# Performance work log

Measured on AMD Instinct MI355X. Metric: run time of the kernel, lower is better.

The kernel has to match this reference:

```python
import jax, jax.numpy as jnp
import numpy as np


def setup_inputs() -> dict:
    key = jax.random.key(0)
    k1, k2, k3 = jax.random.split(key, 3)
    B, S = 4096, 4096
    prediction = jax.random.normal(k1, (B, S), dtype=jnp.float32)
    target = jax.random.normal(k2, (B, S), dtype=jnp.float32)
    mask = jax.random.randint(k3, (B, S), 0, 2, dtype=jnp.int32)
    return {"prediction": prediction, "target": target, "mask": mask}


def reference(prediction, target, mask):
    # Masked MSE with ragged alignment: for each row, the j-th masked position
    # of `prediction` is compared against target[i, j] (i.e. target[:lens[i]]).
    m = mask != 0  # ignored_index == 0
    # rank of each masked position within its row -> index into target row
    rank = jnp.cumsum(m.astype(jnp.int32), axis=1) - 1  # [B, S]
    gathered_target = jnp.take_along_axis(target, jnp.clip(rank, 0, None), axis=1)
    diff2 = jnp.where(m, (prediction - gathered_target) ** 2, jnp.zeros((), prediction.dtype))
    return diff2.sum()  # reduction='sum'
```

## Files before the change

kernel.cpp:

```cpp
#include <hip/hip_runtime.h>

__global__ __launch_bounds__(256) void masked_mse_rows(
    const float* __restrict__ pred,
    const float* __restrict__ target,
    const int*   __restrict__ mask,
    float*       __restrict__ row_sums,
    int S)
{
    const int row  = blockIdx.x;
    const int tid  = threadIdx.x;
    const int lane = tid & 63;
    const int wid  = tid >> 6;

    const float4* __restrict__ p4 = reinterpret_cast<const float4*>(pred + (size_t)row * S);
    const int4*   __restrict__ m4 = reinterpret_cast<const int4*>(mask + (size_t)row * S);
    const float*  __restrict__ trow = target + (size_t)row * S;

    __shared__ int   wsum[4];
    __shared__ float facc[4];

    float acc = 0.0f;
    int running = 0;
    const int nchunk = S >> 10;

    for (int c = 0; c < nchunk; ++c) {
        const int idx = c * 256 + tid;
        const int4   m = m4[idx];
        const float4 p = p4[idx];

        const int b0 = (m.x != 0), b1 = (m.y != 0), b2 = (m.z != 0), b3 = (m.w != 0);
        const int cnt = b0 + b1 + b2 + b3;

        int scan = cnt;
        #pragma unroll
        for (int off = 1; off < 64; off <<= 1) {
            int n = __shfl_up(scan, off, 64);
            if (lane >= off) scan += n;
        }
        if (lane == 63) wsum[wid] = scan;
        __syncthreads();

        int wave_off = 0;
        #pragma unroll
        for (int w = 0; w < 4; ++w) wave_off += (w < wid) ? wsum[w] : 0;
        const int total = wsum[0] + wsum[1] + wsum[2] + wsum[3];

        int r = running + wave_off + (scan - cnt);

        if (b0) { float d = p.x - trow[r]; acc += d * d; ++r; }
        if (b1) { float d = p.y - trow[r]; acc += d * d; ++r; }
        if (b2) { float d = p.z - trow[r]; acc += d * d; ++r; }
        if (b3) { float d = p.w - trow[r]; acc += d * d; ++r; }

        running += total;
        __syncthreads();
    }

    #pragma unroll
    for (int off = 32; off > 0; off >>= 1) acc += __shfl_down(acc, off, 64);
    if (lane == 0) facc[wid] = acc;
    __syncthreads();
    if (tid == 0) row_sums[row] = facc[0] + facc[1] + facc[2] + facc[3];
}

__global__ __launch_bounds__(256) void reduce_rows(
    const float* __restrict__ row_sums, float* __restrict__ out, int n)
{
    const int tid = threadIdx.x;
    float acc = 0.0f;
    for (int i = tid; i < n; i += 256) acc += row_sums[i];
    #pragma unroll
    for (int off = 32; off > 0; off >>= 1) acc += __shfl_down(acc, off, 64);
    __shared__ float facc[4];
    if ((tid & 63) == 0) facc[tid >> 6] = acc;
    __syncthreads();
    if (tid == 0) out[0] = facc[0] + facc[1] + facc[2] + facc[3];
}

extern "C" void kernel_launch(void* const* d_in, const int* in_sizes, int n_in,
                              void* d_out, int out_size, void* d_ws, size_t ws_size,
                              hipStream_t stream) {
    const float* pred   = (const float*)d_in[0];
    const float* target = (const float*)d_in[1];
    const int*   mask   = (const int*)d_in[2];
    float* out = (float*)d_out;
    float* row_sums = (float*)d_ws;

    const int S = 4096;
    const int B = in_sizes[0] / S;

    masked_mse_rows<<<B, 256, 0, stream>>>(pred, target, mask, row_sums, S);
    reduce_rows<<<1, 256, 0, stream>>>(row_sums, out, B);
}
```

Before: 36.15 us.

## Assign one row per wavefront to remove block-level scan barriers

Each 64-lane wavefront now processes a whole row, so the prefix-sum offset comes only from the in-wave shuffle scan plus a broadcast of lane 63. This drops the shared-memory wave-sum exchange and both __syncthreads per chunk. Each lane also loads two float4/int4 vectors per iteration with unroll 2, giving more memory requests in flight. In exchange, each row's scan runs serially within one wave over more iterations, and the grid has a quarter as many blocks.

```diff
diff --git a/kernel.cpp b/kernel.cpp
--- a/kernel.cpp
+++ b/kernel.cpp
@@ -5,31 +5,33 @@
     const float* __restrict__ target,
     const int*   __restrict__ mask,
     float*       __restrict__ row_sums,
-    int S)
+    int S, int B)
 {
-    const int row  = blockIdx.x;
     const int tid  = threadIdx.x;
     const int lane = tid & 63;
     const int wid  = tid >> 6;
+    const int row  = blockIdx.x * 4 + wid;
+    if (row >= B) return;
 
     const float4* __restrict__ p4 = reinterpret_cast<const float4*>(pred + (size_t)row * S);
     const int4*   __restrict__ m4 = reinterpret_cast<const int4*>(mask + (size_t)row * S);
     const float*  __restrict__ trow = target + (size_t)row * S;
 
-    __shared__ int   wsum[4];
-    __shared__ float facc[4];
-
     float acc = 0.0f;
     int running = 0;
-    const int nchunk = S >> 10;
+    const int niter = S >> 9;
 
-    for (int c = 0; c < nchunk; ++c) {
-        const int idx = c * 256 + tid;
-        const int4   m = m4[idx];
-        const float4 p = p4[idx];
+    #pragma unroll 2
+    for (int it = 0; it < niter; ++it) {
+        const int base = it * 128 + lane * 2;
+        const int4   ma = m4[base];
+        const int4   mb = m4[base + 1];
+        const float4 pa = p4[base];
+        const float4 pb = p4[base + 1];
 
-        const int b0 = (m.x != 0), b1 = (m.y != 0), b2 = (m.z != 0), b3 = (m.w != 0);
-        const int cnt = b0 + b1 + b2 + b3;
+        const int b0 = (ma.x != 0), b1 = (ma.y != 0), b2 = (ma.z != 0), b3 = (ma.w != 0);
+        const int b4 = (mb.x != 0), b5 = (mb.y != 0), b6 = (mb.z != 0), b7 = (mb.w != 0);
+        const int cnt = b0 + b1 + b2 + b3 + b4 + b5 + b6 + b7;
 
         int scan = cnt;
         #pragma unroll
@@ -37,30 +39,24 @@
             int n = __shfl_up(scan, off, 64);
             if (lane >= off) scan += n;
         }
-        if (lane == 63) wsum[wid] = scan;
-        __syncthreads();
 
-        int wave_off = 0;
-        #pragma unroll
-        for (int w = 0; w < 4; ++w) wave_off += (w < wid) ? wsum[w] : 0;
-        const int total = wsum[0] + wsum[1] + wsum[2] + wsum[3];
+        int r = running + (scan - cnt);
 
-        int r = running + wave_off + (scan - cnt);
+        if (b0) { float d = pa.x - trow[r]; acc += d * d; ++r; }
+        if (b1) { float d = pa.y - trow[r]; acc += d * d; ++r; }
+        if (b2) { float d = pa.z - trow[r]; acc += d * d; ++r; }
+        if (b3) { float d = pa.w - trow[r]; acc += d * d; ++r; }
+        if (b4) { float d = pb.x - trow[r]; acc += d * d; ++r; }
+        if (b5) { float d = pb.y - trow[r]; acc += d * d; ++r; }
+        if (b6) { float d = pb.z - trow[r]; acc += d * d; ++r; }
+        if (b7) { float d = pb.w - trow[r]; acc += d * d; ++r; }
 
-        if (b0) { float d = p.x - trow[r]; acc += d * d; ++r; }
-        if (b1) { float d = p.y - trow[r]; acc += d * d; ++r; }
-        if (b2) { float d = p.z - trow[r]; acc += d * d; ++r; }
-        if (b3) { float d = p.w - trow[r]; acc += d * d; ++r; }
-
-        running += total;
-        __syncthreads();
+        running += __shfl(scan, 63, 64);
     }
 
     #pragma unroll
     for (int off = 32; off > 0; off >>= 1) acc += __shfl_down(acc, off, 64);
-    if (lane == 0) facc[wid] = acc;
-    __syncthreads();
-    if (tid == 0) row_sums[row] = facc[0] + facc[1] + facc[2] + facc[3];
+    if (lane == 0) row_sums[row] = acc;
 }
 
 __global__ __launch_bounds__(256) void reduce_rows(
@@ -89,6 +85,6 @@
     const int S = 4096;
     const int B = in_sizes[0] / S;
 
-    masked_mse_rows<<<B, 256, 0, stream>>>(pred, target, mask, row_sums, S);
+    masked_mse_rows<<<(B + 3) / 4, 256, 0, stream>>>(pred, target, mask, row_sums, S, B);
     reduce_rows<<<1, 256, 0, stream>>>(row_sums, out, B);
 }
```

Result: slower. 41.38 us (+14.5%).

## Replace per-chunk shuffle scan with ballot/mbcnt prefix and single block sync

Applied to the files above, without the earlier changes.

The row kernel now uses 512 threads that each load two float4/int4 chunks up front. It computes per-lane prefix counts with ballot and mbcnt instead of a 6-step shuffle scan inside a 4-iteration loop. This cuts the number of block-wide barriers from eight to two and issues all loads early for more memory-level parallelism. The final reduction kernel uses 1024 threads with float4 loads. Register pressure rises because two chunks are held per thread, and the occupancy hint of 8 blocks may constrain register allocation.

```diff
diff --git a/kernel.cpp b/kernel.cpp
--- a/kernel.cpp
+++ b/kernel.cpp
@@ -1,80 +1,110 @@
 #include <hip/hip_runtime.h>
 
-__global__ __launch_bounds__(256) void masked_mse_rows(
+__device__ __forceinline__ int lanes_below(unsigned long long m) {
+    return __builtin_amdgcn_mbcnt_hi((unsigned)(m >> 32),
+           __builtin_amdgcn_mbcnt_lo((unsigned)m, 0u));
+}
+
+__global__ __launch_bounds__(512, 8) void masked_mse_rows(
     const float* __restrict__ pred,
     const float* __restrict__ target,
     const int*   __restrict__ mask,
     float*       __restrict__ row_sums,
     int S)
 {
-    const int row  = blockIdx.x;
     const int tid  = threadIdx.x;
     const int lane = tid & 63;
     const int wid  = tid >> 6;
+    const int row  = blockIdx.x;
 
     const float4* __restrict__ p4 = reinterpret_cast<const float4*>(pred + (size_t)row * S);
     const int4*   __restrict__ m4 = reinterpret_cast<const int4*>(mask + (size_t)row * S);
     const float*  __restrict__ trow = target + (size_t)row * S;
 
-    __shared__ int   wsum[4];
-    __shared__ float facc[4];
+    const int4   ma = m4[tid];
+    const int4   mb = m4[tid + 512];
+    const float4 pa = p4[tid];
+    const float4 pb = p4[tid + 512];
+
+    const unsigned long long a0 = __ballot(ma.x != 0);
+    const unsigned long long a1 = __ballot(ma.y != 0);
+    const unsigned long long a2 = __ballot(ma.z != 0);
+    const unsigned long long a3 = __ballot(ma.w != 0);
+    const unsigned long long b0 = __ballot(mb.x != 0);
+    const unsigned long long b1 = __ballot(mb.y != 0);
+    const unsigned long long b2 = __ballot(mb.z != 0);
+    const unsigned long long b3 = __ballot(mb.w != 0);
+
+    const int pref_a = lanes_below(a0) + lanes_below(a1) + lanes_below(a2) + lanes_below(a3);
+    const int pref_b = lanes_below(b0) + lanes_below(b1) + lanes_below(b2) + lanes_below(b3);
+    const int tot_a  = __popcll(a0) + __popcll(a1) + __popcll(a2) + __popcll(a3);
+    const int tot_b  = __popcll(b0) + __popcll(b1) + __popcll(b2) + __popcll(b3);
+
+    __shared__ int   ta[8], tb[8];
+    __shared__ float facc[8];
+    if (lane == 0) { ta[wid] = tot_a; tb[wid] = tot_b; }
+    __syncthreads();
+
+    int woff_a = 0, base_b = 0, woff_b = 0;
+    #pragma unroll
+    for (int w = 0; w < 8; ++w) {
+        woff_a += (w < wid) ? ta[w] : 0;
+        base_b += ta[w];
+        woff_b += (w < wid) ? tb[w] : 0;
+    }
 
     float acc = 0.0f;
-    int running = 0;
-    const int nchunk = S >> 10;
-
-    for (int c = 0; c < nchunk; ++c) {
-        const int idx = c * 256 + tid;
-        const int4   m = m4[idx];
-        const float4 p = p4[idx];
-
-        const int b0 = (m.x != 0), b1 = (m.y != 0), b2 = (m.z != 0), b3 = (m.w != 0);
-        const int cnt = b0 + b1 + b2 + b3;
-
-        int scan = cnt;
-        #pragma unroll
-        for (int off = 1; off < 64; off <<= 1) {
-            int n = __shfl_up(scan, off, 64);
-            if (lane >= off) scan += n;
-        }
-        if (lane == 63) wsum[wid] = scan;
-        __syncthreads();
-
-        int wave_off = 0;
-        #pragma unroll
-        for (int w = 0; w < 4; ++w) wave_off += (w < wid) ? wsum[w] : 0;
-        const int total = wsum[0] + wsum[1] + wsum[2] + wsum[3];
-
-        int r = running + wave_off + (scan - cnt);
-
-        if (b0) { float d = p.x - trow[r]; acc += d * d; ++r; }
-        if (b1) { float d = p.y - trow[r]; acc += d * d; ++r; }
-        if (b2) { float d = p.z - trow[r]; acc += d * d; ++r; }
-        if (b3) { float d = p.w - trow[r]; acc += d * d; ++r; }
-
-        running += total;
-        __syncthreads();
+    {
+        int r = woff_a + pref_a;
+        if (ma.x != 0) { float d = pa.x - trow[r]; acc += d * d; ++r; }
+        if (ma.y != 0) { float d = pa.y - trow[r]; acc += d * d; ++r; }
+        if (ma.z != 0) { float d = pa.z - trow[r]; acc += d * d; ++r; }
+        if (ma.w != 0) { float d = pa.w - trow[r]; acc += d * d; ++r; }
+    }
+    {
+        int r = base_b + woff_b + pref_b;
+        if (mb.x != 0) { float d = pb.x - trow[r]; acc += d * d; ++r; }
+        if (mb.y != 0) { float d = pb.y - trow[r]; acc += d * d; ++r; }
+        if (mb.z != 0) { float d = pb.z - trow[r]; acc += d * d; ++r; }
+        if (mb.w != 0) { float d = pb.w - trow[r]; acc += d * d; ++r; }
     }
 
     #pragma unroll
     for (int off = 32; off > 0; off >>= 1) acc += __shfl_down(acc, off, 64);
     if (lane == 0) facc[wid] = acc;
     __syncthreads();
-    if (tid == 0) row_sums[row] = facc[0] + facc[1] + facc[2] + facc[3];
+    if (tid == 0) {
+        float s = 0.0f;
+        #pragma unroll
+        for (int w = 0; w < 8; ++w) s += facc[w];
+        row_sums[row] = s;
+    }
 }
 
-__global__ __launch_bounds__(256) void reduce_rows(
+__global__ __launch_bounds__(1024) void reduce_rows(
     const float* __restrict__ row_sums, float* __restrict__ out, int n)
 {
     const int tid = threadIdx.x;
     float acc = 0.0f;
-    for (int i = tid; i < n; i += 256) acc += row_sums[i];
+    const int n4 = n >> 2;
+    const float4* rs4 = reinterpret_cast<const float4*>(row_sums);
+    for (int i = tid; i < n4; i += 1024) {
+        float4 v = rs4[i];
+        acc += (v.x + v.y) + (v.z + v.w);
+    }
+    for (int i = (n4 << 2) + tid; i < n; i += 1024) acc += row_sums[i];
+
     #pragma unroll
     for (int off = 32; off > 0; off >>= 1) acc += __shfl_down(acc, off, 64);
-    __shared__ float facc[4];
+    __shared__ float facc[16];
     if ((tid & 63) == 0) facc[tid >> 6] = acc;
     __syncthreads();
-    if (tid == 0) out[0] = facc[0] + facc[1] + facc[2] + facc[3];
+    if (tid == 0) {
+        float s = 0.0f;
+        #pragma unroll
+        for (int w = 0; w < 16; ++w) s += facc[w];
+        out[0] = s;
+    }
 }
 
 extern "C" void kernel_launch(void* const* d_in, const int* in_sizes, int n_in,
@@ -89,6 +119,6 @@
     const int S = 4096;
     const int B = in_sizes[0] / S;
 
-    masked_mse_rows<<<B, 256, 0, stream>>>(pred, target, mask, row_sums, S);
-    reduce_rows<<<1, 256, 0, stream>>>(row_sums, out, B);
+    masked_mse_rows<<<B, 512, 0, stream>>>(pred, target, mask, row_sums, S);
+    reduce_rows<<<1, 1024, 0, stream>>>(row_sums, out, B);
 }
```

Result: faster. 35.27 us (-2.4%).
